# Kernel optimization log

Measured on AMD Instinct MI355X. Metric: run time of the kernel, lower is better.

## Reference

```python
import jax, jax.numpy as jnp
import numpy as np

M, NQ, NK = 2, 1024, 1024
DX, DT = 256, 2
H, D = 8, 32          # num_heads, head_dim
KH = 32               # kernel MLP hidden width
SCALE = D ** -0.5


def setup_inputs() -> dict:
    key = jax.random.key(0)
    ks = jax.random.split(key, 16)
    p = 0.02
    return {
        "xq": jax.random.normal(ks[0], (M, NQ, DX), jnp.float32),
        "xk": jax.random.normal(ks[1], (M, NK, DX), jnp.float32),
        "xv": jax.random.normal(ks[2], (M, NK, DX), jnp.float32),
        "tq": jax.random.normal(ks[3], (M, NQ, DT), jnp.float32),
        "tk": jax.random.normal(ks[4], (M, NK, DT), jnp.float32),
        # projections (no bias, as in nn.Linear(..., bias=False))
        "Wq": jax.random.normal(ks[5], (DX, H * D), jnp.float32) * p,
        "Wk": jax.random.normal(ks[6], (DX, H * D), jnp.float32) * p,
        "Wv": jax.random.normal(ks[7], (DX, H * D), jnp.float32) * p,
        # output projection (with bias)
        "Wo": jax.random.normal(ks[8], (H * D, DX), jnp.float32) * p,
        "bo": jnp.zeros((DX,), jnp.float32),
        # kernel MLP: dt -> KH -> H
        "Wk1": jax.random.normal(ks[9], (DT, KH), jnp.float32) * 0.5,
        "bk1": jnp.zeros((KH,), jnp.float32),
        "Wk2": jax.random.normal(ks[10], (KH, H), jnp.float32) * 0.5,
        "bk2": jnp.zeros((H,), jnp.float32),
        # phi_t: H -> DT
        "Wphi": jax.random.normal(ks[11], (H, DT), jnp.float32) * p,
        "bphi": jnp.zeros((DT,), jnp.float32),
    }


def reference(xq, xk, xv, tq, tk, Wq, Wk, Wv, Wo, bo, Wk1, bk1, Wk2, bk2, Wphi, bphi):
    m, nq, _ = xq.shape
    nk = xk.shape[1]
    # translation group action: diff [m, nq, nk, dt]
    diff = tq[:, :, None, :] - tk[:, None, :, :]
    # q, k: [m, h, n, d]
    q = (xq @ Wq).reshape(m, nq, H, D).transpose(0, 2, 1, 3)
    k = (xk @ Wk).reshape(m, nk, H, D).transpose(0, 2, 1, 3)
    token_dots = jnp.einsum("bhqd,bhkd->bhqk", q, k) * SCALE
    # kernel MLP bias evaluated densely over diffs -> [m, nq, nk, h] -> [m, h, nq, nk]
    hdn = jax.nn.relu(diff @ Wk1 + bk1)
    kdots = (hdn @ Wk2 + bk2).transpose(0, 3, 1, 2)
    dots = kdots + token_dots
    attn = jax.nn.softmax(dots, axis=-1)  # [m, h, nq, nk]
    v = (xv @ Wv).reshape(m, nk, H, D).transpose(0, 2, 1, 3)
    out = jnp.einsum("bhqk,bhkd->bhqd", attn, v)
    out = out.transpose(0, 2, 1, 3).reshape(m, nq, H * D)
    out = out @ Wo + bo  # dropout p=0
    # phi_t path: attn -> [m, nq, nk, h] -> per-pair dt weights
    attn_t = attn.transpose(0, 2, 3, 1)
    t_dots = attn_t @ Wphi + bphi  # [m, nq, nk, dt]
    tq_new = tq + (1.0 / nk) * jnp.sum(diff * t_dots, axis=-2)
    return out, tq_new
```

## Files before the change

### kernel.cpp

```cpp
#include <hip/hip_runtime.h>
#include <hip/hip_bf16.h>

#define MB 2
#define NQ 1024
#define NK 1024
#define DXC 256
#define HD 256
#define HH 8
#define DD 32
#define KHC 32
#define LOG2E 1.4426950408889634f
#define QSCALE 0.25503472301046627f

#define QB 32
#define KB 32
#define KSPLIT 8
#define KL 128
#define NCHUNK 4

#define QPB_F   0u
#define KPB_F   262144u
#define VPT_F   524288u
#define WT_F    786432u
#define AQH_F   917504u
#define BKH_F   950272u
#define TS_F    983040u
#define TKX_F   983048u
#define W2T_F   986120u
#define PART_F  986376u

typedef float f32x4 __attribute__((ext_vector_type(4)));
typedef short bf16x8 __attribute__((ext_vector_type(8)));
typedef _Float16 f16x8 __attribute__((ext_vector_type(8)));
typedef _Float16 f16x2 __attribute__((ext_vector_type(2)));

#define MFMA(a, b, c)   __builtin_amdgcn_mfma_f32_16x16x32_bf16(a, b, c, 0, 0, 0)
#define MFMA16(a, b, c) __builtin_amdgcn_mfma_f32_16x16x32_f16(a, b, c, 0, 0, 0)
#define EXP2(x) exp2f(x)

#define KDQ 36
#define KDH 1160
#define SMEM_BYTES 28800

struct Ptrs {
    const float *xq, *xk, *xv, *tq, *tk;
    const float *Wq, *Wk, *Wv, *Wo, *bo;
    const float *Wk1, *bk1, *Wk2, *bk2, *Wphi, *bphi;
    float* wsf;
    float* out;
};

__device__ __forceinline__ uint cvt_pk_bf16(float lo, float hi) {
    uint r;
    asm("v_cvt_pk_bf16_f32 %0, %1, %2" : "=v"(r) : "v"(lo), "v"(hi));
    return r;
}
__device__ __forceinline__ ushort f2bf1(float f) { return (ushort)cvt_pk_bf16(f, 0.f); }
__device__ __forceinline__ float bf2f(uint x) {
    return __uint_as_float((x & 0xffffu) << 16);
}
__device__ __forceinline__ ushort f2h(float f) {
    _Float16 h = (_Float16)f;
    return __builtin_bit_cast(ushort, h);
}

__global__ __launch_bounds__(256, 4) void k_phase1(Ptrs p) {
    __shared__ __align__(16) float sW[64][65];
    const int u = blockIdx.x;
    const int t = threadIdx.x;
    ushort* wt  = (ushort*)(p.wsf + WT_F);
    ushort* aqh = (ushort*)(p.wsf + AQH_F);
    ushort* bkh = (ushort*)(p.wsf + BKH_F);
    ushort* tkx = (ushort*)(p.wsf + TKX_F);
    ushort* w2t = (ushort*)(p.wsf + W2T_F);
    float*  ts  = p.wsf + TS_F;

    if (u < 64) {
        const int mat = u >> 4;
        const float* W = (mat == 0) ? p.Wq : (mat == 1) ? p.Wk : (mat == 2) ? p.Wv : p.Wo;
        const int k0 = (u & 3) * 64, c0 = ((u >> 2) & 3) * 64;
        #pragma unroll
        for (int i = 0; i < 4; ++i) {
            int flat = i * 1024 + t * 4;
            int r = flat >> 6, c = flat & 63;
            float4 v4 = *(const float4*)(W + (size_t)(k0 + r) * 256 + c0 + c);
            sW[r][c] = v4.x; sW[r][c + 1] = v4.y; sW[r][c + 2] = v4.z; sW[r][c + 3] = v4.w;
        }
        __syncthreads();
        #pragma unroll
        for (int i = 0; i < 4; ++i) {
            int flat = i * 1024 + t * 4;
            int cc = flat >> 6, kk = flat & 63;
            uint2 pk;
            pk.x = cvt_pk_bf16(sW[kk][cc], sW[kk + 1][cc]);
            pk.y = cvt_pk_bf16(sW[kk + 2][cc], sW[kk + 3][cc]);
            *(uint2*)(wt + (size_t)mat * 65536 + (size_t)(c0 + cc) * 256 + k0 + kk) = pk;
        }
    } else if (u < 320) {
        int gid = (u - 64) * 256 + t;
        int row = gid >> 5, j = gid & 31;
        aqh[gid] = f2h(p.tq[row * 2] * p.Wk1[j] + p.tq[row * 2 + 1] * p.Wk1[KHC + j] + p.bk1[j]);
        bkh[gid] = f2h(p.tk[row * 2] * p.Wk1[j] + p.tk[row * 2 + 1] * p.Wk1[KHC + j]);
    } else if (u < 344) {
        int g = (u - 320) * 256 + t;
        int mm = g / 3072, rr = (g % 3072) >> 10, kk = g & 1023;
        float v = (rr == 0) ? p.tk[(size_t)(mm * NK + kk) * 2]
                : (rr == 1) ? p.tk[(size_t)(mm * NK + kk) * 2 + 1] : 1.0f;
        tkx[g] = f2bf1(v);
    } else if (u == 344) {
        for (int g = t; g < 512; g += 256) {
            int hh2 = g >> 5, jj = g & 31;
            w2t[g] = f2h(hh2 < HH ? p.Wk2[jj * HH + hh2] * LOG2E : 0.f);
        }
    } else {
        const int m = u - 345;
        const int c = t & 1, kk = t >> 1;
        float s = 0.f;
        #pragma unroll
        for (int i = 0; i < 8; ++i) s += p.tk[(size_t)(m * NK + kk + i * 128) * 2 + c];
        float* red = (float*)&sW[0][0];
        red[t] = s; __syncthreads();
        for (int off = 128; off >= 2; off >>= 1) {
            if (t < off) red[t] += red[t + off];
            __syncthreads();
        }
        if (t < 2) ts[m * 2 + t] = red[t];
    }
}

__global__ __launch_bounds__(256, 4) void k_phase2(Ptrs p) {
    __shared__ __align__(16) ushort sTr[256][24];
    const int u = blockIdx.x;
    const int t = threadIdx.x;
    ushort* qpb = (ushort*)(p.wsf + QPB_F);
    ushort* kpb = (ushort*)(p.wsf + KPB_F);
    ushort* vpt = (ushort*)(p.wsf + VPT_F);
    const ushort* wt = (const ushort*)(p.wsf + WT_F);

    const int z = u / 128;
    const int R0 = (u % 128) * 16;
    const float* x = (z == 0) ? p.xq : (z == 1) ? p.xk : p.xv;
    const ushort* wz = wt + (size_t)z * 65536;
    const int wid = t >> 6, l = t & 63, g = l >> 4, c16 = l & 15;
    const int wc = wid * 64;
    const int row = R0 + c16;

    f32x4 acc[4];
    #pragma unroll
    for (int i = 0; i < 4; ++i) acc[i] = (f32x4){0.f, 0.f, 0.f, 0.f};

    for (int k0 = 0; k0 < DXC; k0 += 32) {
        const float* xr = x + (size_t)row * DXC + k0 + g * 8;
        float4 a0 = *(const float4*)xr;
        float4 a1 = *(const float4*)(xr + 4);
        union { bf16x8 v; uint d[4]; } af;
        af.d[0] = cvt_pk_bf16(a0.x, a0.y);
        af.d[1] = cvt_pk_bf16(a0.z, a0.w);
        af.d[2] = cvt_pk_bf16(a1.x, a1.y);
        af.d[3] = cvt_pk_bf16(a1.z, a1.w);
        #pragma unroll
        for (int cf = 0; cf < 4; ++cf) {
            bf16x8 bf = *(const bf16x8*)(wz + (size_t)(wc + cf * 16 + c16) * 256 + k0 + g * 8);
            acc[cf] = MFMA(af.v, bf, acc[cf]);
        }
    }
    if (z != 2) {
        #pragma unroll
        for (int cf = 0; cf < 4; ++cf) {
            #pragma unroll
            for (int r = 0; r < 4; ++r) {
                int orow = R0 + g * 4 + r;
                int col = wc + cf * 16 + c16;
                float v = acc[cf][r];
                if (z == 0) qpb[(size_t)orow * HD + col] = f2bf1(v * QSCALE);
                else        kpb[(size_t)orow * HD + col] = f2bf1(v);
            }
        }
    } else {
        #pragma unroll
        for (int cf = 0; cf < 4; ++cf)
            #pragma unroll
            for (int r = 0; r < 4; ++r)
                sTr[wc + cf * 16 + c16][g * 4 + r] = f2bf1(acc[cf][r]);
        __syncthreads();
        const int mq = R0 >> 10, rin = R0 & 1023;
        ushort* dst = vpt + (size_t)mq * (HD * NK) + (size_t)t * NK + rin;
        *(uint4*)dst       = *(const uint4*)&sTr[t][0];
        *(uint4*)(dst + 8) = *(const uint4*)&sTr[t][8];
    }
}

__global__ __launch_bounds__(256, 2) void k_phase3(Ptrs p) {
    __shared__ __align__(16) char smem[SMEM_BYTES];
    const int u = blockIdx.x;
    const int t = threadIdx.x;

    const ushort* qpb = (const ushort*)(p.wsf + QPB_F);
    const ushort* kpb = (const ushort*)(p.wsf + KPB_F);
    const ushort* vpt = (const ushort*)(p.wsf + VPT_F);
    const ushort* aqh = (const ushort*)(p.wsf + AQH_F);
    const ushort* bkh = (const ushort*)(p.wsf + BKH_F);
    const ushort* tkx = (const ushort*)(p.wsf + TKX_F);
    const ushort* w2t = (const ushort*)(p.wsf + W2T_F);
    ushort* part = (ushort*)(p.wsf + PART_F);

    const int ks = u & 7;
    const int qt = (u >> 3) & 31;
    const int m  = u >> 8;
    const int q0 = qt * QB;
    const int kbase = ks * KL;
    const int wid = t >> 6;
    const int l = t & 63;
    const int g = l >> 4;
    const int c16 = l & 15;

    ushort* sKD = (ushort*)smem;
    ushort (*sP)[32][40] = (ushort(*)[32][40])(smem + 18560);

    f16x8 w2v = *(const f16x8*)(w2t + c16 * 32 + g * 8);
    const float b2l = (c16 < HH) ? p.bk2[c16] * LOG2E : 0.f;
    const f16x8 zero8 = {0, 0, 0, 0, 0, 0, 0, 0};

    bf16x8 qb[2][2];
    #pragma unroll
    for (int hh = 0; hh < 2; ++hh)
        #pragma unroll
        for (int qf = 0; qf < 2; ++qf)
            qb[hh][qf] = *(const bf16x8*)(qpb + (size_t)(m * NQ + q0 + qf * 16 + c16) * HD
                                              + (wid * 2 + hh) * DD + g * 8);
    f16x8 aqv[8];
    #pragma unroll
    for (int qi = 0; qi < 8; ++qi)
        aqv[qi] = *(const f16x8*)(aqh + (size_t)(m * NQ + q0 + wid * 8 + qi) * KHC + g * 8);

    struct ChunkOps {
        f16x8 bk0, bk1;
        bf16x8 ka0[2], ka1[2], v0[2], v1[2];
        bf16x8 vt;
    };
    const size_t vbase = (size_t)m * (HD * NK);
    const size_t tbase = (size_t)m * 3072 + (size_t)(c16 < 2 ? c16 : 2) * NK;
    auto loadChunk = [&](int k0) {
        ChunkOps c;
        c.bk0 = *(const f16x8*)(bkh + (size_t)(m * NK + k0 + c16) * KHC + g * 8);
        c.bk1 = *(const f16x8*)(bkh + (size_t)(m * NK + k0 + 16 + c16) * KHC + g * 8);
        #pragma unroll
        for (int hh = 0; hh < 2; ++hh) {
            const int h = wid * 2 + hh;
            c.ka0[hh] = *(const bf16x8*)(kpb + (size_t)(m * NK + k0 + c16) * HD + h * DD + g * 8);
            c.ka1[hh] = *(const bf16x8*)(kpb + (size_t)(m * NK + k0 + 16 + c16) * HD + h * DD + g * 8);
            c.v0[hh]  = *(const bf16x8*)(vpt + vbase + (size_t)(h * DD + c16) * NK + k0 + g * 8);
            c.v1[hh]  = *(const bf16x8*)(vpt + vbase + (size_t)(h * DD + 16 + c16) * NK + k0 + g * 8);
        }
        c.vt = *(const bf16x8*)(tkx + tbase + k0 + g * 8);
        return c;
    };

    f32x4 oacc[2][2][3];
    #pragma unroll
    for (int a = 0; a < 2; ++a)
        #pragma unroll
        for (int bb = 0; bb < 2; ++bb)
            #pragma unroll
            for (int c = 0; c < 3; ++c)
                oacc[a][bb][c] = (f32x4){0.f, 0.f, 0.f, 0.f};

    ChunkOps cur = loadChunk(kbase);
    for (int ch = 0; ch < NCHUNK; ++ch) {
        ChunkOps nxt;
        if (ch + 1 < NCHUNK) nxt = loadChunk(kbase + (ch + 1) * KB);

        {
            #pragma unroll
            for (int qi = 0; qi < 8; ++qi) {
                const int q = wid * 8 + qi;
                #pragma unroll
                for (int kh = 0; kh < 2; ++kh) {
                    f16x8 d = aqv[qi] - (kh ? cur.bk1 : cur.bk0);
                    f16x8 hv = __builtin_elementwise_max(d, zero8);
                    f32x4 c = {b2l, b2l, b2l, b2l};
                    c = MFMA16(hv, w2v, c);
                    if (c16 < HH) {
                        uint2 st;
                        st.x = __builtin_bit_cast(uint, __builtin_amdgcn_cvt_pkrtz(c[0], c[1]));
                        st.y = __builtin_bit_cast(uint, __builtin_amdgcn_cvt_pkrtz(c[2], c[3]));
                        *(uint2*)&sKD[c16 * KDH + q * KDQ + kh * 16 + g * 4] = st;
                    }
                }
            }
        }
        __syncthreads();

        #pragma unroll
        for (int hh = 0; hh < 2; ++hh) {
            const int h = wid * 2 + hh;
            const ushort* kdb = &sKD[h * KDH];
            #pragma unroll
            for (int kf = 0; kf < 2; ++kf) {
                #pragma unroll
                for (int qf = 0; qf < 2; ++qf) {
                    uint2 kd2 = *(const uint2*)&kdb[(qf * 16 + c16) * KDQ + kf * 16 + g * 4];
                    f16x2 k01 = __builtin_bit_cast(f16x2, kd2.x);
                    f16x2 k23 = __builtin_bit_cast(f16x2, kd2.y);
                    f32x4 cinit = {(float)k01[0], (float)k01[1], (float)k23[0], (float)k23[1]};
                    f32x4 s = MFMA((kf ? cur.ka1[hh] : cur.ka0[hh]), qb[hh][qf], cinit);
                    uint2 pk;
                    pk.x = cvt_pk_bf16(EXP2(s[0]), EXP2(s[1]));
                    pk.y = cvt_pk_bf16(EXP2(s[2]), EXP2(s[3]));
                    *(uint2*)&sP[wid][qf * 16 + c16][kf * 16 + g * 4] = pk;
                }
            }
            #pragma unroll
            for (int qf = 0; qf < 2; ++qf) {
                bf16x8 pa = *(const bf16x8*)&sP[wid][qf * 16 + c16][g * 8];
                oacc[hh][qf][0] = MFMA(pa, cur.v0[hh], oacc[hh][qf][0]);
                oacc[hh][qf][1] = MFMA(pa, cur.v1[hh], oacc[hh][qf][1]);
                oacc[hh][qf][2] = MFMA(pa, cur.vt, oacc[hh][qf][2]);
            }
        }
        __syncthreads();
        if (ch + 1 < NCHUNK) cur = nxt;
    }

    #pragma unroll
    for (int hh = 0; hh < 2; ++hh) {
        int mh = m * HH + wid * 2 + hh;
        #pragma unroll
        for (int qf = 0; qf < 2; ++qf) {
            #pragma unroll
            for (int r = 0; r < 4; ++r) {
                int q = q0 + qf * 16 + g * 4 + r;
                ushort* pb = part + ((size_t)(mh * KSPLIT + ks) * NQ + q) * 40;
                pb[c16]      = f2bf1(oacc[hh][qf][0][r]);
                pb[16 + c16] = f2bf1(oacc[hh][qf][1][r]);
                float e = oacc[hh][qf][2][r];
                if (c16 < 2) pb[32 + c16] = f2bf1(e);
                else if (c16 == 2) *(float*)(pb + 34) = e;
            }
        }
    }
}

__global__ __launch_bounds__(256, 4) void k_phase4(Ptrs p) {
    __shared__ __align__(16) ushort sHob[16][264];
    __shared__ float sD[8][16][2];
    const int u = blockIdx.x;
    const int t = threadIdx.x;
    const ushort* part = (const ushort*)(p.wsf + PART_F);
    const ushort* wt = (const ushort*)(p.wsf + WT_F);
    const float* ts = p.wsf + TS_F;
    float* tq_out = p.out + (size_t)MB * NQ * HD;

    const int m = u >> 6;
    const int q0 = (u & 63) * 16;
    const int h = t >> 5, dgrp = (t >> 4) & 1, qloc = t & 15;
    const int q = q0 + qloc;
    const int mh = m * HH + h;

    float accO[16] = {};
    float aT = 0.f, lsum = 0.f;
    for (int s = 0; s < KSPLIT; ++s) {
        const ushort* ps = part + ((size_t)(mh * KSPLIT + s) * NQ + q) * 40;
        uint4 v0 = *(const uint4*)(ps + dgrp * 16);
        uint4 v1 = *(const uint4*)(ps + dgrp * 16 + 8);
        accO[0] += bf2f(v0.x); accO[1] += bf2f(v0.x >> 16);
        accO[2] += bf2f(v0.y); accO[3] += bf2f(v0.y >> 16);
        accO[4] += bf2f(v0.z); accO[5] += bf2f(v0.z >> 16);
        accO[6] += bf2f(v0.w); accO[7] += bf2f(v0.w >> 16);
        accO[8] += bf2f(v1.x); accO[9] += bf2f(v1.x >> 16);
        accO[10] += bf2f(v1.y); accO[11] += bf2f(v1.y >> 16);
        accO[12] += bf2f(v1.z); accO[13] += bf2f(v1.z >> 16);
        accO[14] += bf2f(v1.w); accO[15] += bf2f(v1.w >> 16);
        uint at = *(const uint*)(ps + 32);
        aT += bf2f(dgrp == 0 ? at : (at >> 16));
        lsum += *(const float*)(ps + 34);
    }
    const float inv = 1.f / lsum;
    {
        uint dd[8];
        #pragma unroll
        for (int i = 0; i < 8; ++i)
            dd[i] = cvt_pk_bf16(accO[2 * i] * inv, accO[2 * i + 1] * inv);
        ushort* hp = &sHob[qloc][h * DD + dgrp * 16];
        *(uint4*)hp       = (uint4){dd[0], dd[1], dd[2], dd[3]};
        *(uint4*)(hp + 8) = (uint4){dd[4], dd[5], dd[6], dd[7]};
    }
    const float A = aT * inv;
    const float tqc = p.tq[(size_t)(m * NQ + q) * 2 + dgrp];
    sD[h][qloc][dgrp] = p.Wphi[h * 2 + dgrp] * (tqc - A);
    __syncthreads();

    if (t < 32) {
        int ql2 = t >> 1, c = t & 1;
        float s = 0.f;
        #pragma unroll
        for (int hh2 = 0; hh2 < 8; ++hh2) s += sD[hh2][ql2][c];
        int qg = q0 + ql2;
        float tqv = p.tq[(size_t)(m * NQ + qg) * 2 + c];
        const float invnk = 1.f / (float)NK;
        tq_out[(size_t)(m * NQ + qg) * 2 + c] =
            tqv + s * invnk + p.bphi[c] * (tqv - ts[m * 2 + c] * invnk);
    }

    const ushort* wz3 = wt + (size_t)3 * 65536;
    const int wid = t >> 6, l = t & 63, g = l >> 4, c16 = l & 15;
    f32x4 acc[4];
    #pragma unroll
    for (int i = 0; i < 4; ++i) acc[i] = (f32x4){0.f, 0.f, 0.f, 0.f};
    for (int k0 = 0; k0 < HD; k0 += 32) {
        bf16x8 af = *(const bf16x8*)&sHob[c16][k0 + g * 8];
        #pragma unroll
        for (int cf = 0; cf < 4; ++cf) {
            int col = wid * 64 + cf * 16 + c16;
            bf16x8 bf = *(const bf16x8*)(wz3 + (size_t)col * 256 + k0 + g * 8);
            acc[cf] = MFMA(af, bf, acc[cf]);
        }
    }
    #pragma unroll
    for (int cf = 0; cf < 4; ++cf) {
        int col = wid * 64 + cf * 16 + c16;
        float bv = p.bo[col];
        #pragma unroll
        for (int r = 0; r < 4; ++r) {
            int orow = q0 + g * 4 + r;
            p.out[(size_t)(m * NQ + orow) * DXC + col] = acc[cf][r] + bv;
        }
    }
}

extern "C" void kernel_launch(void* const* d_in, const int* in_sizes, int n_in,
                              void* d_out, int out_size, void* d_ws, size_t ws_size,
                              hipStream_t stream)
{
    Ptrs p;
    p.xq   = (const float*)d_in[0];
    p.xk   = (const float*)d_in[1];
    p.xv   = (const float*)d_in[2];
    p.tq   = (const float*)d_in[3];
    p.tk   = (const float*)d_in[4];
    p.Wq   = (const float*)d_in[5];
    p.Wk   = (const float*)d_in[6];
    p.Wv   = (const float*)d_in[7];
    p.Wo   = (const float*)d_in[8];
    p.bo   = (const float*)d_in[9];
    p.Wk1  = (const float*)d_in[10];
    p.bk1  = (const float*)d_in[11];
    p.Wk2  = (const float*)d_in[12];
    p.bk2  = (const float*)d_in[13];
    p.Wphi = (const float*)d_in[14];
    p.bphi = (const float*)d_in[15];
    p.wsf  = (float*)d_ws;
    p.out  = (float*)d_out;

    hipLaunchKernelGGL(k_phase1, dim3(347), dim3(256), 0, stream, p);
    hipLaunchKernelGGL(k_phase2, dim3(384), dim3(256), 0, stream, p);
    hipLaunchKernelGGL(k_phase3, dim3(512), dim3(256), 0, stream, p);
    hipLaunchKernelGGL(k_phase4, dim3(128), dim3(256), 0, stream, p);
}
```

Baseline: 56.90 us.

## Double-buffer kernel-MLP bias tile to overlap next chunk with QK/PV

```diff
diff --git a/kernel.cpp b/kernel.cpp
--- a/kernel.cpp
+++ b/kernel.cpp
@@ -40,7 +40,6 @@
 
 #define KDQ 36
 #define KDH 1160
-#define SMEM_BYTES 28800
 
 struct Ptrs {
     const float *xq, *xk, *xv, *tq, *tk;
@@ -191,7 +190,7 @@
 }
 
 __global__ __launch_bounds__(256, 2) void k_phase3(Ptrs p) {
-    __shared__ __align__(16) char smem[SMEM_BYTES];
+    __shared__ __align__(16) char smem[47360];
     const int u = blockIdx.x;
     const int t = threadIdx.x;
 
@@ -214,8 +213,9 @@
     const int g = l >> 4;
     const int c16 = l & 15;
 
-    ushort* sKD = (ushort*)smem;
-    ushort (*sP)[32][40] = (ushort(*)[32][40])(smem + 18560);
+    ushort* KD0 = (ushort*)smem;
+    ushort* KD1 = (ushort*)(smem + 18560);
+    ushort (*sP)[32][40] = (ushort(*)[32][40])(smem + 37120);
 
     f16x8 w2v = *(const f16x8*)(w2t + c16 * 32 + g * 8);
     const float b2l = (c16 < HH) ? p.bk2[c16] * LOG2E : 0.f;
@@ -233,17 +233,19 @@
     for (int qi = 0; qi < 8; ++qi)
         aqv[qi] = *(const f16x8*)(aqh + (size_t)(m * NQ + q0 + wid * 8 + qi) * KHC + g * 8);
 
-    struct ChunkOps {
-        f16x8 bk0, bk1;
-        bf16x8 ka0[2], ka1[2], v0[2], v1[2];
-        bf16x8 vt;
-    };
+    struct BkOps { f16x8 b0, b1; };
+    struct KavOps { bf16x8 ka0[2], ka1[2], v0[2], v1[2], vt; };
     const size_t vbase = (size_t)m * (HD * NK);
     const size_t tbase = (size_t)m * 3072 + (size_t)(c16 < 2 ? c16 : 2) * NK;
-    auto loadChunk = [&](int k0) {
-        ChunkOps c;
-        c.bk0 = *(const f16x8*)(bkh + (size_t)(m * NK + k0 + c16) * KHC + g * 8);
-        c.bk1 = *(const f16x8*)(bkh + (size_t)(m * NK + k0 + 16 + c16) * KHC + g * 8);
+
+    auto loadBk = [&](int k0) {
+        BkOps c;
+        c.b0 = *(const f16x8*)(bkh + (size_t)(m * NK + k0 + c16) * KHC + g * 8);
+        c.b1 = *(const f16x8*)(bkh + (size_t)(m * NK + k0 + 16 + c16) * KHC + g * 8);
+        return c;
+    };
+    auto loadKav = [&](int k0) {
+        KavOps c;
         #pragma unroll
         for (int hh = 0; hh < 2; ++hh) {
             const int h = wid * 2 + hh;
@@ -265,36 +267,30 @@
             for (int c = 0; c < 3; ++c)
                 oacc[a][bb][c] = (f32x4){0.f, 0.f, 0.f, 0.f};
 
-    ChunkOps cur = loadChunk(kbase);
-    for (int ch = 0; ch < NCHUNK; ++ch) {
-        ChunkOps nxt;
-        if (ch + 1 < NCHUNK) nxt = loadChunk(kbase + (ch + 1) * KB);
-
-        {
-            #pragma unroll
-            for (int qi = 0; qi < 8; ++qi) {
-                const int q = wid * 8 + qi;
-                #pragma unroll
-                for (int kh = 0; kh < 2; ++kh) {
-                    f16x8 d = aqv[qi] - (kh ? cur.bk1 : cur.bk0);
-                    f16x8 hv = __builtin_elementwise_max(d, zero8);
-                    f32x4 c = {b2l, b2l, b2l, b2l};
-                    c = MFMA16(hv, w2v, c);
-                    if (c16 < HH) {
-                        uint2 st;
-                        st.x = __builtin_bit_cast(uint, __builtin_amdgcn_cvt_pkrtz(c[0], c[1]));
-                        st.y = __builtin_bit_cast(uint, __builtin_amdgcn_cvt_pkrtz(c[2], c[3]));
-                        *(uint2*)&sKD[c16 * KDH + q * KDQ + kh * 16 + g * 4] = st;
-                    }
+    auto kdPhase = [&](const BkOps& bk, ushort* kdb) {
+        #pragma unroll
+        for (int qi = 0; qi < 8; ++qi) {
+            const int q = wid * 8 + qi;
+            #pragma unroll
+            for (int kh = 0; kh < 2; ++kh) {
+                f16x8 d = aqv[qi] - (kh ? bk.b1 : bk.b0);
+                f16x8 hv = __builtin_elementwise_max(d, zero8);
+                f32x4 c = {b2l, b2l, b2l, b2l};
+                c = MFMA16(hv, w2v, c);
+                if (c16 < HH) {
+                    uint2 st;
+                    st.x = __builtin_bit_cast(uint, __builtin_amdgcn_cvt_pkrtz(c[0], c[1]));
+                    st.y = __builtin_bit_cast(uint, __builtin_amdgcn_cvt_pkrtz(c[2], c[3]));
+                    *(uint2*)&kdb[c16 * KDH + q * KDQ + kh * 16 + g * 4] = st;
                 }
             }
         }
-        __syncthreads();
-
+    };
+    auto qkpv = [&](const KavOps& kv, const ushort* kdbuf) {
         #pragma unroll
         for (int hh = 0; hh < 2; ++hh) {
             const int h = wid * 2 + hh;
-            const ushort* kdb = &sKD[h * KDH];
+            const ushort* kdb = &kdbuf[h * KDH];
             #pragma unroll
             for (int kf = 0; kf < 2; ++kf) {
                 #pragma unroll
@@ -303,7 +299,7 @@
                     f16x2 k01 = __builtin_bit_cast(f16x2, kd2.x);
                     f16x2 k23 = __builtin_bit_cast(f16x2, kd2.y);
                     f32x4 cinit = {(float)k01[0], (float)k01[1], (float)k23[0], (float)k23[1]};
-                    f32x4 s = MFMA((kf ? cur.ka1[hh] : cur.ka0[hh]), qb[hh][qf], cinit);
+                    f32x4 s = MFMA((kf ? kv.ka1[hh] : kv.ka0[hh]), qb[hh][qf], cinit);
                     uint2 pk;
                     pk.x = cvt_pk_bf16(EXP2(s[0]), EXP2(s[1]));
                     pk.y = cvt_pk_bf16(EXP2(s[2]), EXP2(s[3]));
@@ -313,14 +309,34 @@
             #pragma unroll
             for (int qf = 0; qf < 2; ++qf) {
                 bf16x8 pa = *(const bf16x8*)&sP[wid][qf * 16 + c16][g * 8];
-                oacc[hh][qf][0] = MFMA(pa, cur.v0[hh], oacc[hh][qf][0]);
-                oacc[hh][qf][1] = MFMA(pa, cur.v1[hh], oacc[hh][qf][1]);
-                oacc[hh][qf][2] = MFMA(pa, cur.vt, oacc[hh][qf][2]);
+                oacc[hh][qf][0] = MFMA(pa, kv.v0[hh], oacc[hh][qf][0]);
+                oacc[hh][qf][1] = MFMA(pa, kv.v1[hh], oacc[hh][qf][1]);
+                oacc[hh][qf][2] = MFMA(pa, kv.vt, oacc[hh][qf][2]);
             }
         }
-        __syncthreads();
-        if (ch + 1 < NCHUNK) cur = nxt;
-    }
+    };
+
+    BkOps bk0v = loadBk(kbase);
+    KavOps kv0 = loadKav(kbase);
+    BkOps bk1v = loadBk(kbase + KB);
+    KavOps kv1 = loadKav(kbase + KB);
+    kdPhase(bk0v, KD0);
+    __syncthreads();
+
+    kdPhase(bk1v, KD1);
+    BkOps bk2v = loadBk(kbase + 2 * KB);
+    qkpv(kv0, KD0);
+    kv0 = loadKav(kbase + 2 * KB);
+    __syncthreads();
+    kdPhase(bk2v, KD0);
+    BkOps bk3v = loadBk(kbase + 3 * KB);
+    qkpv(kv1, KD1);
+    kv1 = loadKav(kbase + 3 * KB);
+    __syncthreads();
+    kdPhase(bk3v, KD1);
+    qkpv(kv0, KD0);
+    __syncthreads();
+    qkpv(kv1, KD1);
 
     #pragma unroll
     for (int hh = 0; hh < 2; ++hh) {
```

Result: no change. 56.34 us (-1.0%).
